# Kernel optimization log

Measured on AMD Instinct MI355X. Metric: run time of the kernel, lower is better.

## Reference

```python
import jax, jax.numpy as jnp
import numpy as np

B, D, M, P, I, O = 256, 10, 32, 36, 8, 16
NUM_ITERATIONS = 3
EPS = 1e-07


def squash(s, axis=-1):
    sq = jnp.sum(s * s, axis=axis, keepdims=True)
    safe_norm = jnp.sqrt(sq + EPS)
    scale = sq / (1.0 + sq)
    return scale * (s / safe_norm)


def setup_inputs() -> dict:
    key = jax.random.key(0)
    kx, kw = jax.random.split(key)
    x = jax.random.normal(kx, (B, M, P, I), dtype=jnp.float32)
    # Parameter shape matches torch: [1, D, M, 1, O, I]
    W = 0.01 * jax.random.normal(kw, (1, D, M, 1, O, I), dtype=jnp.float32)
    return {"x": x, "W": W}


def reference(x, W):
    Wd = W[0, :, :, 0]  # [D, M, O, I]
    # u_hat: [B, D, M, P, O]
    u_hat = jnp.einsum('dmoi,bmpi->bdmpo', Wd, x)
    tu = jax.lax.stop_gradient(u_hat)
    b = jnp.zeros(u_hat.shape[:4], dtype=u_hat.dtype)  # [B, D, M, P]
    for _ in range(NUM_ITERATIONS - 1):
        c = jax.nn.softmax(b, axis=1)                 # over digit caps
        s = jnp.einsum('bdmp,bdmpo->bdo', c, tu)
        v = squash(s)
        b = b + jnp.einsum('bdmpo,bdo->bdmp', tu, v)
    # Final softmax over dim=3 (primary-cap axis), faithful to source
    c = jax.nn.softmax(b, axis=3)
    s = jnp.einsum('bdmp,bdmpo->bdo', c, u_hat)
    return squash(s)
```

## Files before the change

### kernel.cpp

```cpp
#include <hip/hip_runtime.h>
#include <math.h>

#define BB 256
#define DD 10
#define MM 32
#define PP 36
#define II 8
#define OO 16
#define NT 640
#define XS 292
#define RS 37

__device__ __forceinline__ float dot8(const float4 a0, const float4 a1,
                                      const float4 b0, const float4 b1) {
    return a0.x*b0.x + a0.y*b0.y + a0.z*b0.z + a0.w*b0.w
         + a1.x*b1.x + a1.y*b1.y + a1.z*b1.z + a1.w*b1.w;
}

__global__ void __launch_bounds__(NT) caps_routing(
    const float* __restrict__ x,
    const float* __restrict__ W,
    float* __restrict__ out)
{
    const int bidx = blockIdx.x;
    const int tid  = threadIdx.x;
    const int wave = tid >> 6;
    const int lane = tid & 63;
    const float* __restrict__ xb = x + (size_t)bidx * (MM*PP*II);

    __shared__ __align__(16) float xs  [MM*XS];
    __shared__ __align__(16) float z   [DD*MM*II];
    __shared__ __align__(16) float y   [DD*MM*II];
    __shared__ __align__(16) float ybar[MM*II];
    __shared__ __align__(16) float rinv[MM*RS];

    {
        const float4* xg = (const float4*)xb;
        #pragma unroll
        for (int k = 0; k < 4; ++k) {
            const int t = tid + k*NT;
            if (t < MM*72) {
                const int m = t / 72, r = t - m*72;
                *(float4*)(xs + m*XS + 4*r) = xg[t];
            }
        }
        if (tid < MM*II) {
            const int m = tid >> 3, i = tid & 7;
            const float* xr = xb + m*(PP*II) + i;
            float acc = 0.f;
            #pragma unroll 6
            for (int p = 0; p < PP; ++p) acc += xr[p*II];
            ybar[tid] = 0.1f * acc;
        }
    }
    __syncthreads();

    {
        const int d = wave;
        const int o = lane & 15, q = lane >> 4;
        float s1 = 0.f;
        #pragma unroll
        for (int j = 0; j < 8; ++j) {
            const int m = q*8 + j;
            const float4* wp = (const float4*)(W + ((size_t)((d*MM + m)*OO + o)) * II);
            const float4* yp = (const float4*)(ybar + m*II);
            s1 += dot8(wp[0], wp[1], yp[0], yp[1]);
        }
        s1 += __shfl_xor(s1, 16, 64);
        s1 += __shfl_xor(s1, 32, 64);
        float sq = s1 * s1;
        sq += __shfl_xor(sq, 1, 64);
        sq += __shfl_xor(sq, 2, 64);
        sq += __shfl_xor(sq, 4, 64);
        sq += __shfl_xor(sq, 8, 64);
        const float v1 = (sq / (1.f + sq)) * (s1 / sqrtf(sq + 1e-7f));
        float vv[OO];
        #pragma unroll
        for (int o2 = 0; o2 < OO; ++o2) vv[o2] = __shfl(v1, o2, 64);
        #pragma unroll
        for (int k = 0; k < 4; ++k) {
            const int mi = k*64 + lane;
            const int m = mi >> 3, i = mi & 7;
            const float* wp = W + ((size_t)(d*MM + m)*OO) * II + i;
            float acc = 0.f;
            #pragma unroll
            for (int o2 = 0; o2 < OO; ++o2) acc += wp[o2*II] * vv[o2];
            z[d*(MM*II) + mi] = acc;
        }
    }
    __syncthreads();

    #pragma unroll
    for (int k = 0; k < 2; ++k) {
        const int t = tid + k*NT;
        if (t < MM*PP) {
            const int m = t / PP, p = t - m*PP;
            const float4* xp = (const float4*)(xs + m*XS + p*II);
            const float4 x0 = xp[0], x1 = xp[1];
            float se = 0.f;
            #pragma unroll
            for (int d2 = 0; d2 < DD; ++d2) {
                const float4* zp = (const float4*)(z + (d2*MM + m)*II);
                se += __expf(dot8(x0, x1, zp[0], zp[1]));
            }
            rinv[m*RS + p] = 1.0f / se;
        }
    }
    __syncthreads();

    {
        const int d  = wave;
        float* __restrict__ zd = z + d*(MM*II);
        float* __restrict__ yd = y + d*(MM*II);

        const int mL = lane >> 1, ih = lane & 1;
        {
            const float4* zp = (const float4*)(zd + mL*II);
            const float4 z0 = zp[0], z1v = zp[1];
            const float* xr = xs + mL*XS;
            const float* rr = rinv + mL*RS;
            float a0=0.f, a1=0.f, a2=0.f, a3=0.f;
            #pragma unroll 4
            for (int p = 0; p < PP; ++p) {
                const float4* xp = (const float4*)(xr + p*II);
                const float4 x0 = xp[0], x1 = xp[1];
                const float e = __expf(dot8(x0, x1, z0, z1v)) * rr[p];
                const float4 xh = ih ? x1 : x0;
                a0 += e*xh.x; a1 += e*xh.y; a2 += e*xh.z; a3 += e*xh.w;
            }
            *(float4*)(yd + mL*II + ih*4) = make_float4(a0,a1,a2,a3);
        }

        const int o = lane & 15, q = lane >> 4;
        float s2 = 0.f;
        #pragma unroll
        for (int j = 0; j < 8; ++j) {
            const int m = q*8 + j;
            const float4* wp = (const float4*)(W + ((size_t)((d*MM + m)*OO + o)) * II);
            const float4* yp = (const float4*)(yd + m*II);
            s2 += dot8(wp[0], wp[1], yp[0], yp[1]);
        }
        s2 += __shfl_xor(s2, 16, 64);
        s2 += __shfl_xor(s2, 32, 64);
        float sq = s2 * s2;
        sq += __shfl_xor(sq, 1, 64);
        sq += __shfl_xor(sq, 2, 64);
        sq += __shfl_xor(sq, 4, 64);
        sq += __shfl_xor(sq, 8, 64);
        const float v2 = (sq / (1.f + sq)) * (s2 / sqrtf(sq + 1e-7f));
        float vv[OO];
        #pragma unroll
        for (int o2 = 0; o2 < OO; ++o2) vv[o2] = __shfl(v2, o2, 64);

        #pragma unroll
        for (int k = 0; k < 4; ++k) {
            const int mi = k*64 + lane;
            const int m = mi >> 3, i = mi & 7;
            const float* wp = W + ((size_t)(d*MM + m)*OO) * II + i;
            float acc = 0.f;
            #pragma unroll
            for (int o2 = 0; o2 < OO; ++o2) acc += wp[o2*II] * vv[o2];
            zd[mi] += acc;
        }

        {
            const float4* zp = (const float4*)(zd + mL*II);
            const float4 z0 = zp[0], z1v = zp[1];
            const float* xr = xs + mL*XS;
            float se = 0.f;
            float a0=0.f, a1=0.f, a2=0.f, a3=0.f;
            #pragma unroll 4
            for (int p = 0; p < PP; ++p) {
                const float4* xp = (const float4*)(xr + p*II);
                const float4 x0 = xp[0], x1 = xp[1];
                const float e = __expf(dot8(x0, x1, z0, z1v));
                se += e;
                const float4 xh = ih ? x1 : x0;
                a0 += e*xh.x; a1 += e*xh.y; a2 += e*xh.z; a3 += e*xh.w;
            }
            const float rs = 1.f / se;
            *(float4*)(yd + mL*II + ih*4) = make_float4(a0*rs, a1*rs, a2*rs, a3*rs);
        }

        float s3 = 0.f;
        #pragma unroll
        for (int j = 0; j < 8; ++j) {
            const int m = q*8 + j;
            const float4* wp = (const float4*)(W + ((size_t)((d*MM + m)*OO + o)) * II);
            const float4* yp = (const float4*)(yd + m*II);
            s3 += dot8(wp[0], wp[1], yp[0], yp[1]);
        }
        s3 += __shfl_xor(s3, 16, 64);
        s3 += __shfl_xor(s3, 32, 64);
        float sq3 = s3 * s3;
        sq3 += __shfl_xor(sq3, 1, 64);
        sq3 += __shfl_xor(sq3, 2, 64);
        sq3 += __shfl_xor(sq3, 4, 64);
        sq3 += __shfl_xor(sq3, 8, 64);
        const float r = (sq3 / (1.f + sq3)) * (s3 / sqrtf(sq3 + 1e-7f));
        if (lane < OO)
            out[(size_t)bidx * (DD*OO) + d*OO + o] = r;
    }
}

extern "C" void kernel_launch(void* const* d_in, const int* in_sizes, int n_in,
                              void* d_out, int out_size, void* d_ws, size_t ws_size,
                              hipStream_t stream) {
    (void)in_sizes; (void)n_in; (void)out_size; (void)d_ws; (void)ws_size;
    const float* x = (const float*)d_in[0];
    const float* W = (const float*)d_in[1];
    float* out = (float*)d_out;
    caps_routing<<<dim3(BB), dim3(NT), 0, stream>>>(x, W, out);
}
```

Before: 78.18 us.

## Split each batch across two blocks of five digit-waves and halve x loads

Launches 512 blocks of 320 threads, with each block covering half of the digit capsules for one batch element. Each block redundantly recomputes the first routing iteration for all ten digits, which is needed for the softmax denominator. The inner routing loops now load only one float4 of x per lane and combine the two half dot products with a shuffle, cutting LDS traffic. The cost is duplicated x loading and first-iteration work across the two blocks, in exchange for more blocks and higher occupancy.

```diff
diff --git a/kernel.cpp b/kernel.cpp
--- a/kernel.cpp
+++ b/kernel.cpp
@@ -7,7 +7,7 @@
 #define PP 36
 #define II 8
 #define OO 16
-#define NT 640
+#define NT 320
 #define XS 292
 #define RS 37
 
@@ -16,13 +16,17 @@
     return a0.x*b0.x + a0.y*b0.y + a0.z*b0.z + a0.w*b0.w
          + a1.x*b1.x + a1.y*b1.y + a1.z*b1.z + a1.w*b1.w;
 }
-
-__global__ void __launch_bounds__(NT) caps_routing(
+__device__ __forceinline__ float dot4(const float4 a, const float4 b) {
+    return a.x*b.x + a.y*b.y + a.z*b.z + a.w*b.w;
+}
+
+__global__ void __launch_bounds__(NT, 3) caps_routing(
     const float* __restrict__ x,
     const float* __restrict__ W,
     float* __restrict__ out)
 {
-    const int bidx = blockIdx.x;
+    const int bidx = blockIdx.x & 255;
+    const int half = blockIdx.x >> 8;
     const int tid  = threadIdx.x;
     const int wave = tid >> 6;
     const int lane = tid & 63;
@@ -30,14 +34,14 @@
 
     __shared__ __align__(16) float xs  [MM*XS];
     __shared__ __align__(16) float z   [DD*MM*II];
-    __shared__ __align__(16) float y   [DD*MM*II];
+    __shared__ __align__(16) float y   [5*MM*II];
     __shared__ __align__(16) float ybar[MM*II];
     __shared__ __align__(16) float rinv[MM*RS];
 
     {
         const float4* xg = (const float4*)xb;
         #pragma unroll
-        for (int k = 0; k < 4; ++k) {
+        for (int k = 0; k < 8; ++k) {
             const int t = tid + k*NT;
             if (t < MM*72) {
                 const int m = t / 72, r = t - m*72;
@@ -56,42 +60,45 @@
     __syncthreads();
 
     {
-        const int d = wave;
         const int o = lane & 15, q = lane >> 4;
-        float s1 = 0.f;
-        #pragma unroll
-        for (int j = 0; j < 8; ++j) {
-            const int m = q*8 + j;
-            const float4* wp = (const float4*)(W + ((size_t)((d*MM + m)*OO + o)) * II);
-            const float4* yp = (const float4*)(ybar + m*II);
-            s1 += dot8(wp[0], wp[1], yp[0], yp[1]);
-        }
-        s1 += __shfl_xor(s1, 16, 64);
-        s1 += __shfl_xor(s1, 32, 64);
-        float sq = s1 * s1;
-        sq += __shfl_xor(sq, 1, 64);
-        sq += __shfl_xor(sq, 2, 64);
-        sq += __shfl_xor(sq, 4, 64);
-        sq += __shfl_xor(sq, 8, 64);
-        const float v1 = (sq / (1.f + sq)) * (s1 / sqrtf(sq + 1e-7f));
-        float vv[OO];
-        #pragma unroll
-        for (int o2 = 0; o2 < OO; ++o2) vv[o2] = __shfl(v1, o2, 64);
-        #pragma unroll
-        for (int k = 0; k < 4; ++k) {
-            const int mi = k*64 + lane;
-            const int m = mi >> 3, i = mi & 7;
-            const float* wp = W + ((size_t)(d*MM + m)*OO) * II + i;
-            float acc = 0.f;
-            #pragma unroll
-            for (int o2 = 0; o2 < OO; ++o2) acc += wp[o2*II] * vv[o2];
-            z[d*(MM*II) + mi] = acc;
+        #pragma unroll
+        for (int r = 0; r < 2; ++r) {
+            const int d = wave + r*5;
+            float s1 = 0.f;
+            #pragma unroll
+            for (int j = 0; j < 8; ++j) {
+                const int m = q*8 + j;
+                const float4* wp = (const float4*)(W + ((size_t)((d*MM + m)*OO + o)) * II);
+                const float4* yp = (const float4*)(ybar + m*II);
+                s1 += dot8(wp[0], wp[1], yp[0], yp[1]);
+            }
+            s1 += __shfl_xor(s1, 16, 64);
+            s1 += __shfl_xor(s1, 32, 64);
+            float sq = s1 * s1;
+            sq += __shfl_xor(sq, 1, 64);
+            sq += __shfl_xor(sq, 2, 64);
+            sq += __shfl_xor(sq, 4, 64);
+            sq += __shfl_xor(sq, 8, 64);
+            const float v1 = (sq / (1.f + sq)) * (s1 / sqrtf(sq + 1e-7f));
+            float vv[OO];
+            #pragma unroll
+            for (int o2 = 0; o2 < OO; ++o2) vv[o2] = __shfl(v1, o2, 64);
+            #pragma unroll
+            for (int k = 0; k < 4; ++k) {
+                const int mi = k*64 + lane;
+                const int m = mi >> 3, i = mi & 7;
+                const float* wp = W + ((size_t)(d*MM + m)*OO) * II + i;
+                float acc = 0.f;
+                #pragma unroll
+                for (int o2 = 0; o2 < OO; ++o2) acc += wp[o2*II] * vv[o2];
+                z[d*(MM*II) + mi] = acc;
+            }
         }
     }
     __syncthreads();
 
     #pragma unroll
-    for (int k = 0; k < 2; ++k) {
+    for (int k = 0; k < 4; ++k) {
         const int t = tid + k*NT;
         if (t < MM*PP) {
             const int m = t / PP, p = t - m*PP;
@@ -109,23 +116,23 @@
     __syncthreads();
 
     {
-        const int d  = wave;
+        const int d = half*5 + wave;
         float* __restrict__ zd = z + d*(MM*II);
-        float* __restrict__ yd = y + d*(MM*II);
+        float* __restrict__ yd = y + wave*(MM*II);
 
         const int mL = lane >> 1, ih = lane & 1;
+        const float* xr = xs + mL*XS + ih*4;
+        const float4 zh = *(const float4*)(zd + mL*II + ih*4);
+
         {
-            const float4* zp = (const float4*)(zd + mL*II);
-            const float4 z0 = zp[0], z1v = zp[1];
-            const float* xr = xs + mL*XS;
             const float* rr = rinv + mL*RS;
             float a0=0.f, a1=0.f, a2=0.f, a3=0.f;
             #pragma unroll 4
             for (int p = 0; p < PP; ++p) {
-                const float4* xp = (const float4*)(xr + p*II);
-                const float4 x0 = xp[0], x1 = xp[1];
-                const float e = __expf(dot8(x0, x1, z0, z1v)) * rr[p];
-                const float4 xh = ih ? x1 : x0;
+                const float4 xh = *(const float4*)(xr + p*II);
+                float bh = dot4(xh, zh);
+                bh += __shfl_xor(bh, 1, 64);
+                const float e = __expf(bh) * rr[p];
                 a0 += e*xh.x; a1 += e*xh.y; a2 += e*xh.z; a3 += e*xh.w;
             }
             *(float4*)(yd + mL*II + ih*4) = make_float4(a0,a1,a2,a3);
@@ -164,18 +171,16 @@
         }
 
         {
-            const float4* zp = (const float4*)(zd + mL*II);
-            const float4 z0 = zp[0], z1v = zp[1];
-            const float* xr = xs + mL*XS;
+            const float4 zh2 = *(const float4*)(zd + mL*II + ih*4);
             float se = 0.f;
             float a0=0.f, a1=0.f, a2=0.f, a3=0.f;
             #pragma unroll 4
             for (int p = 0; p < PP; ++p) {
-                const float4* xp = (const float4*)(xr + p*II);
-                const float4 x0 = xp[0], x1 = xp[1];
-                const float e = __expf(dot8(x0, x1, z0, z1v));
+                const float4 xh = *(const float4*)(xr + p*II);
+                float bh = dot4(xh, zh2);
+                bh += __shfl_xor(bh, 1, 64);
+                const float e = __expf(bh);
                 se += e;
-                const float4 xh = ih ? x1 : x0;
                 a0 += e*xh.x; a1 += e*xh.y; a2 += e*xh.z; a3 += e*xh.w;
             }
             const float rs = 1.f / se;
@@ -210,5 +215,5 @@
     const float* x = (const float*)d_in[0];
     const float* W = (const float*)d_in[1];
     float* out = (float*)d_out;
-    caps_routing<<<dim3(BB), dim3(NT), 0, stream>>>(x, W, out);
-}
+    caps_routing<<<dim3(BB*2), dim3(NT), 0, stream>>>(x, W, out);
+}
```

New measurement: 88.81 us. +13.6%, slower.
